# Performance work log

Hardware: AMD Instinct MI355X
Metric: run time of the kernel (lower is better)

## Reference

```python
import jax, jax.numpy as jnp
import numpy as np

B, T, C, H = 4, 2048, 1024, 16
D = C // H          # head_dim = 64
FF = 2 * C          # ff_mult = 2
EPS = 1e-5


def _layernorm(x, g, b):
    mu = jnp.mean(x, axis=-1, keepdims=True)
    var = jnp.mean((x - mu) ** 2, axis=-1, keepdims=True)
    return (x - mu) * jax.lax.rsqrt(var + EPS) * g + b


def setup_inputs() -> dict:
    key = jax.random.key(0)
    ks = jax.random.split(key, 8)
    x = jax.random.normal(ks[0], (B, T, C), dtype=jnp.float32)
    perm = jax.random.permutation(ks[1], T).astype(jnp.int32)
    s_c = 1.0 / np.sqrt(C)
    s_f = 1.0 / np.sqrt(FF)
    Wqkv = jax.random.normal(ks[2], (C, 3 * C), dtype=jnp.float32) * s_c
    Wproj = jax.random.normal(ks[3], (C, C), dtype=jnp.float32) * s_c
    bproj = jnp.zeros((C,), dtype=jnp.float32)
    ln1_g = jnp.ones((C,), dtype=jnp.float32)
    ln1_b = jnp.zeros((C,), dtype=jnp.float32)
    ln2_g = jnp.ones((C,), dtype=jnp.float32)
    ln2_b = jnp.zeros((C,), dtype=jnp.float32)
    Wff1 = jax.random.normal(ks[4], (C, FF), dtype=jnp.float32) * s_c
    bff1 = jnp.zeros((FF,), dtype=jnp.float32)
    Wff2 = jax.random.normal(ks[5], (FF, C), dtype=jnp.float32) * s_f
    bff2 = jnp.zeros((C,), dtype=jnp.float32)
    return {"x": x, "perm": perm, "Wqkv": Wqkv, "Wproj": Wproj, "bproj": bproj,
            "ln1_g": ln1_g, "ln1_b": ln1_b, "ln2_g": ln2_g, "ln2_b": ln2_b,
            "Wff1": Wff1, "bff1": bff1, "Wff2": Wff2, "bff2": bff2}


def reference(x, perm, Wqkv, Wproj, bproj, ln1_g, ln1_b, ln2_g, ln2_b,
              Wff1, bff1, Wff2, bff2):
    # --- attention branch ---
    h = _layernorm(x, ln1_g, ln1_b)                       # [B,T,C]
    qkv = (h @ Wqkv).reshape(B, T, 3, H, D)
    q, k, v = qkv[:, :, 0], qkv[:, :, 1], qkv[:, :, 2]    # [B,T,H,D]
    # random-permuted causal additive mask: masked = ~tril[:, perm]
    rows = jnp.arange(T)[:, None]
    masked = perm[None, :] > rows                          # [T,T] bool
    bias = jnp.where(masked, -jnp.inf, 0.0).astype(x.dtype)
    scale = 1.0 / np.sqrt(D)
    scores = jnp.einsum('bqhd,bkhd->bhqk', q, k) * scale + bias
    attn = jax.nn.softmax(scores, axis=-1)                 # [B,H,T,T]
    y = jnp.einsum('bhqk,bkhd->bqhd', attn, v).reshape(B, T, C)
    x = x + y @ Wproj + bproj
    # --- MLP branch ---
    h2 = _layernorm(x, ln2_g, ln2_b)
    ff = jax.nn.gelu(h2 @ Wff1 + bff1, approximate=False) @ Wff2 + bff2
    return x + ff
```

## Files before the change

### kernel.cpp

```cpp
#include <hip/hip_runtime.h>
#include <math.h>

#define Bb 4
#define Tt 2048
#define Cc 1024
#define Hh 16
#define Dd 64
#define FFf 2048
#define Mrows (Bb*Tt)

typedef _Float16 f16;
typedef _Float16 half8 __attribute__((ext_vector_type(8)));
typedef _Float16 half4 __attribute__((ext_vector_type(4)));
typedef _Float16 half2 __attribute__((ext_vector_type(2)));
typedef float floatx4 __attribute__((ext_vector_type(4)));

#define MFMA16(a,b,c)    __builtin_amdgcn_mfma_f32_16x16x32_f16(a,b,c,0,0,0)
#define MFMA16K16(a,b,c) __builtin_amdgcn_mfma_f32_16x16x16f16(a,b,c,0,0,0)

__device__ __forceinline__ void g2l16(const void* g, void* l) {
  __builtin_amdgcn_global_load_lds((__attribute__((address_space(1))) void*)(g),
                                   (__attribute__((address_space(3))) void*)(l),
                                   16, 0, 0);
}

__global__ __launch_bounds__(256) void wt_all_kernel(
    const float* __restrict__ Wqkv, const float* __restrict__ Wproj,
    const float* __restrict__ Wff1, const float* __restrict__ Wff2,
    f16* __restrict__ WqkvT, f16* __restrict__ WprojT,
    f16* __restrict__ Wff1T, f16* __restrict__ Wff2T) {
  __shared__ float tile[32][33];
  int idx = blockIdx.x;
  const float* W; f16* WT; int K, N, n0, k0;
  if (idx < 3072)      { W = Wqkv;  WT = WqkvT;  K = Cc;  N = 3*Cc; n0 = (idx % 96)*32; k0 = (idx / 96)*32; }
  else if (idx < 4096) { idx -= 3072; W = Wproj; WT = WprojT; K = Cc;  N = Cc;  n0 = (idx % 32)*32; k0 = (idx / 32)*32; }
  else if (idx < 6144) { idx -= 4096; W = Wff1;  WT = Wff1T;  K = Cc;  N = FFf; n0 = (idx % 64)*32; k0 = (idx / 64)*32; }
  else                 { idx -= 6144; W = Wff2;  WT = Wff2T;  K = FFf; N = Cc;  n0 = (idx % 32)*32; k0 = (idx / 32)*32; }
  const int tx = threadIdx.x, ty = threadIdx.y;
  #pragma unroll
  for (int i = 0; i < 4; i++)
    tile[ty + 8*i][tx] = W[(size_t)(k0 + ty + 8*i) * N + n0 + tx];
  __syncthreads();
  #pragma unroll
  for (int i = 0; i < 4; i++)
    WT[(size_t)(n0 + ty + 8*i) * K + k0 + tx] = (f16)tile[tx][ty + 8*i];
}

__global__ __launch_bounds__(256) void ln_kernel(const float* __restrict__ x,
                                                 const float* __restrict__ gam,
                                                 const float* __restrict__ bet,
                                                 f16* __restrict__ out) {
  const int row = blockIdx.x;
  const int tid = threadIdx.x;
  const float4 v = ((const float4*)(x + (size_t)row * Cc))[tid];
  float s  = v.x + v.y + v.z + v.w;
  float ss = v.x*v.x + v.y*v.y + v.z*v.z + v.w*v.w;
  #pragma unroll
  for (int o = 32; o >= 1; o >>= 1) { s += __shfl_xor(s, o); ss += __shfl_xor(ss, o); }
  __shared__ float ps[4], pss[4];
  if ((tid & 63) == 0) { ps[tid >> 6] = s; pss[tid >> 6] = ss; }
  __syncthreads();
  s  = ps[0] + ps[1] + ps[2] + ps[3];
  ss = pss[0] + pss[1] + pss[2] + pss[3];
  const float mu   = s * (1.0f / Cc);
  const float rstd = rsqrtf(ss * (1.0f / Cc) - mu * mu + 1e-5f);
  const float4 g4 = ((const float4*)gam)[tid];
  const float4 b4 = ((const float4*)bet)[tid];
  half4 o;
  o[0] = (f16)((v.x - mu) * rstd * g4.x + b4.x);
  o[1] = (f16)((v.y - mu) * rstd * g4.y + b4.y);
  o[2] = (f16)((v.z - mu) * rstd * g4.z + b4.z);
  o[3] = (f16)((v.w - mu) * rstd * g4.w + b4.w);
  ((half4*)(out + (size_t)row * Cc))[tid] = o;
}

template <int MODE>
__global__ __launch_bounds__(256, 3) void gemm_kernel(
    const f16* __restrict__ A, const f16* __restrict__ Bt, const int Kdim,
    const float* __restrict__ resid, const float* __restrict__ bias,
    float* __restrict__ outF, f16* __restrict__ outH,
    f16* __restrict__ outQ, f16* __restrict__ outK, f16* __restrict__ outV) {
  __shared__ f16 As[128 * 32];
  __shared__ f16 Bs[128 * 32];
  const int tid = threadIdx.x;
  const int lane = tid & 63;
  const int w = tid >> 6;
  const int wr = w >> 1, wc = w & 1;
  const int bm = blockIdx.y, bn = blockIdx.x;

  floatx4 acc[4][4] = {};

  const size_t aBase = (size_t)(bm*128 + w*32 + (lane >> 2)) * Kdim + (lane & 3) * 8;
  const size_t bBase = (size_t)(bn*128 + w*32 + (lane >> 2)) * Kdim + (lane & 3) * 8;

  for (int ks = 0; ks < Kdim; ks += 32) {
    __syncthreads();
    g2l16(A  + aBase + ks,                    &As[(w*2 + 0) * 512]);
    g2l16(A  + aBase + (size_t)16*Kdim + ks,  &As[(w*2 + 1) * 512]);
    g2l16(Bt + bBase + ks,                    &Bs[(w*2 + 0) * 512]);
    g2l16(Bt + bBase + (size_t)16*Kdim + ks,  &Bs[(w*2 + 1) * 512]);
    __syncthreads();
    half8 aF[4], bF[4];
    #pragma unroll
    for (int mi = 0; mi < 4; mi++)
      aF[mi] = *(const half8*)&As[(wr*64 + mi*16 + (lane & 15)) * 32 + (lane >> 4) * 8];
    #pragma unroll
    for (int ni = 0; ni < 4; ni++)
      bF[ni] = *(const half8*)&Bs[(wc*64 + ni*16 + (lane & 15)) * 32 + (lane >> 4) * 8];
    #pragma unroll
    for (int mi = 0; mi < 4; mi++)
      #pragma unroll
      for (int ni = 0; ni < 4; ni++)
        acc[mi][ni] = MFMA16(aF[mi], bF[ni], acc[mi][ni]);
  }

  const int rowBase = bm*128 + wr*64;
  const int colBase = bn*128 + wc*64;
  const int quadL = (lane >> 4);
  #pragma unroll
  for (int mi = 0; mi < 4; mi++) {
    #pragma unroll
    for (int ni = 0; ni < 4; ni++) {
      const int col = colBase + ni*16 + (lane & 15);
      if (MODE == 0) {
        const int s = col >> 10;
        const int hh = (col >> 6) & 15;
        const int d = col & 63;
        const int row0 = rowBase + mi*16 + quadL*4;
        const int bI = row0 >> 11;
        const int t0 = row0 & 2047;
        if (s == 2) {
          const size_t addr = (((size_t)(bI*Hh + hh)) * Dd + d) * Tt +
                              (t0 & ~63) + quadL*16 + ((t0 >> 4) & 3) * 4;
          half4 o;
          #pragma unroll
          for (int r = 0; r < 4; r++) o[r] = (f16)acc[mi][ni][r];
          *(half4*)&outV[addr] = o;
        } else {
          f16* dst = (s == 0) ? outQ : outK;
          const float sc = (s == 0) ? 0.18033688f : 1.0f;
          #pragma unroll
          for (int r = 0; r < 4; r++)
            dst[(((size_t)(bI*Hh + hh)) * Tt + t0 + r) * Dd + d] = (f16)(acc[mi][ni][r] * sc);
        }
      } else {
        #pragma unroll
        for (int r = 0; r < 4; r++) {
          const int row = rowBase + mi*16 + quadL*4 + r;
          const float vv = acc[mi][ni][r];
          if (MODE == 1) {
            const size_t a = (size_t)row * Cc + col;
            outF[a] = vv + resid[a] + bias[col];
          } else if (MODE == 2) {
            const float t = vv + bias[col];
            const float gl = 0.5f * t * (1.0f + erff(t * 0.70710678118654752f));
            outH[(size_t)row * FFf + col] = (f16)gl;
          } else {
            const size_t a = (size_t)row * Cc + col;
            outF[a] = vv + bias[col] + resid[a];
          }
        }
      }
    }
  }
}

__global__ __launch_bounds__(256, 4) void attn_kernel(
    const f16* __restrict__ Q, const f16* __restrict__ Kg,
    const f16* __restrict__ Vtp, const int* __restrict__ perm,
    f16* __restrict__ Y) {
  __shared__ f16 Ks[64 * 64];
  __shared__ f16 Vs[64 * 64];
  __shared__ int permS[64];

  const int tid = threadIdx.x;
  const int lane = tid & 63;
  const int w = tid >> 6;
  const int low = lane & 15;
  const int quad = lane >> 4;
  const int bh = blockIdx.y;
  const int q0 = blockIdx.x * 128;
  const int b = bh >> 4, h = bh & 15;

  half8 qF[2][2];
  {
    const size_t base = ((size_t)bh * Tt + q0 + w*32) * Dd;
    #pragma unroll
    for (int qi = 0; qi < 2; qi++)
      #pragma unroll
      for (int kc = 0; kc < 2; kc++)
        qF[qi][kc] = *(const half8*)(Q + base + (size_t)(qi*16 + low) * Dd +
                                     kc*32 + quad*8);
  }

  floatx4 O[4][2] = {};
  floatx4 Ol[2] = {};
  const half4 ones4 = {(f16)1.f, (f16)1.f, (f16)1.f, (f16)1.f};

  const int gd = ((lane & 7) ^ (lane >> 3)) * 8;
  const int krow = lane >> 3;

  for (int kt = 0; kt < Tt / 64; kt++) {
    const int kbase = kt * 64;
    __syncthreads();
    {
      const size_t kgBase = ((size_t)bh * Tt + kbase) * Dd;
      const size_t vgBase = ((size_t)bh * Dd) * Tt + kbase;
      g2l16(Kg  + kgBase + (size_t)(w*16 + 0 + krow) * Dd + gd, &Ks[(w*2 + 0) * 512]);
      g2l16(Kg  + kgBase + (size_t)(w*16 + 8 + krow) * Dd + gd, &Ks[(w*2 + 1) * 512]);
      g2l16(Vtp + vgBase + (size_t)(w*16 + 0 + krow) * Tt + gd, &Vs[(w*2 + 0) * 512]);
      g2l16(Vtp + vgBase + (size_t)(w*16 + 8 + krow) * Tt + gd, &Vs[(w*2 + 1) * 512]);
      if (tid < 64) permS[tid] = perm[kbase + tid];
    }
    __syncthreads();

    floatx4 S[2][4] = {};
    #pragma unroll
    for (int kc = 0; kc < 2; kc++) {
      #pragma unroll
      for (int ki = 0; ki < 4; ki++) {
        const int key = ki*16 + low;
        const half8 kf = *(const half8*)&Ks[key * 64 + (((kc*4 + quad) ^ (lane & 7)) * 8)];
        S[0][ki] = MFMA16(kf, qF[0][kc], S[0][ki]);
        S[1][ki] = MFMA16(kf, qF[1][kc], S[1][ki]);
      }
    }

    int4 pk[4];
    #pragma unroll
    for (int ki = 0; ki < 4; ki++) pk[ki] = *(const int4*)&permS[ki*16 + quad*4];

    half4 pF[2][4];
    #pragma unroll
    for (int qi = 0; qi < 2; qi++) {
      const int qrow = q0 + w*32 + qi*16 + low;
      #pragma unroll
      for (int ki = 0; ki < 4; ki++) {
        const floatx4 sv = S[qi][ki];
        const float p0 = (pk[ki].x > qrow) ? 0.f : __builtin_amdgcn_exp2f(sv[0]);
        const float p1 = (pk[ki].y > qrow) ? 0.f : __builtin_amdgcn_exp2f(sv[1]);
        const float p2 = (pk[ki].z > qrow) ? 0.f : __builtin_amdgcn_exp2f(sv[2]);
        const float p3 = (pk[ki].w > qrow) ? 0.f : __builtin_amdgcn_exp2f(sv[3]);
        const half2 lo = __builtin_bit_cast(half2, __builtin_amdgcn_cvt_pkrtz(p0, p1));
        const half2 hi = __builtin_bit_cast(half2, __builtin_amdgcn_cvt_pkrtz(p2, p3));
        pF[qi][ki] = __builtin_shufflevector(lo, hi, 0, 1, 2, 3);
      }
    }

    #pragma unroll
    for (int ki2 = 0; ki2 < 2; ki2++) {
      Ol[0] = MFMA16K16(ones4, pF[0][2*ki2 + 0], Ol[0]);
      Ol[1] = MFMA16K16(ones4, pF[1][2*ki2 + 0], Ol[1]);
      Ol[0] = MFMA16K16(ones4, pF[0][2*ki2 + 1], Ol[0]);
      Ol[1] = MFMA16K16(ones4, pF[1][2*ki2 + 1], Ol[1]);
      #pragma unroll
      for (int ni = 0; ni < 4; ni++) {
        const int d = ni*16 + low;
        const half8 v8 = *(const half8*)&Vs[d * 64 + (((quad*2 + ki2) ^ (lane & 7)) * 8)];
        const half4 vfA = __builtin_shufflevector(v8, v8, 0, 1, 2, 3);
        const half4 vfB = __builtin_shufflevector(v8, v8, 4, 5, 6, 7);
        O[ni][0] = MFMA16K16(vfA, pF[0][2*ki2 + 0], O[ni][0]);
        O[ni][1] = MFMA16K16(vfA, pF[1][2*ki2 + 0], O[ni][1]);
        O[ni][0] = MFMA16K16(vfB, pF[0][2*ki2 + 1], O[ni][0]);
        O[ni][1] = MFMA16K16(vfB, pF[1][2*ki2 + 1], O[ni][1]);
      }
    }
  }

  #pragma unroll
  for (int qi = 0; qi < 2; qi++) {
    const float linv = 1.0f / Ol[qi][0];
    const int trow = q0 + w*32 + qi*16 + low;
    #pragma unroll
    for (int ni = 0; ni < 4; ni++) {
      half4 o;
      #pragma unroll
      for (int r = 0; r < 4; r++) o[r] = (f16)(O[ni][qi][r] * linv);
      *(half4*)&Y[((size_t)(b * Tt + trow)) * Cc + h*64 + ni*16 + quad*4] = o;
    }
  }
}

extern "C" void kernel_launch(void* const* d_in, const int* in_sizes, int n_in,
                              void* d_out, int out_size, void* d_ws, size_t ws_size,
                              hipStream_t stream) {
  const float* x     = (const float*)d_in[0];
  const int*   perm  = (const int*)d_in[1];
  const float* Wqkv  = (const float*)d_in[2];
  const float* Wproj = (const float*)d_in[3];
  const float* bproj = (const float*)d_in[4];
  const float* ln1g  = (const float*)d_in[5];
  const float* ln1b  = (const float*)d_in[6];
  const float* ln2g  = (const float*)d_in[7];
  const float* ln2b  = (const float*)d_in[8];
  const float* Wff1  = (const float*)d_in[9];
  const float* bff1  = (const float*)d_in[10];
  const float* Wff2  = (const float*)d_in[11];
  const float* bff2  = (const float*)d_in[12];
  float* out = (float*)d_out;

  char* ws = (char*)d_ws;
  size_t off = 0;
  auto alloc = [&](size_t bytes) -> void* {
    void* p = ws + off;
    off += (bytes + 255) & ~(size_t)255;
    return p;
  };
  f16*   h1     = (f16*)alloc((size_t)Mrows * Cc * 2);
  f16*   qb     = (f16*)alloc((size_t)Mrows * Cc * 2);
  f16*   kb     = (f16*)alloc((size_t)Mrows * Cc * 2);
  f16*   vtp    = (f16*)alloc((size_t)Mrows * Cc * 2);
  f16*   yb     = (f16*)alloc((size_t)Mrows * Cc * 2);
  float* xa     = (float*)alloc((size_t)Mrows * Cc * 4);
  f16*   h2     = (f16*)alloc((size_t)Mrows * Cc * 2);
  f16*   gb     = (f16*)alloc((size_t)Mrows * FFf * 2);
  f16*   WqkvT  = (f16*)alloc((size_t)3 * Cc * Cc * 2);
  f16*   WprojT = (f16*)alloc((size_t)Cc * Cc * 2);
  f16*   Wff1T  = (f16*)alloc((size_t)FFf * Cc * 2);
  f16*   Wff2T  = (f16*)alloc((size_t)Cc * FFf * 2);

  wt_all_kernel<<<8192, dim3(32, 8), 0, stream>>>(Wqkv, Wproj, Wff1, Wff2,
                                                  WqkvT, WprojT, Wff1T, Wff2T);

  ln_kernel<<<Mrows, 256, 0, stream>>>(x, ln1g, ln1b, h1);

  gemm_kernel<0><<<dim3(3*Cc/128, Mrows/128), 256, 0, stream>>>(
      h1, WqkvT, Cc, nullptr, nullptr, nullptr, nullptr, qb, kb, vtp);

  attn_kernel<<<dim3(Tt/128, Bb*Hh), 256, 0, stream>>>(qb, kb, vtp, perm, yb);

  gemm_kernel<1><<<dim3(Cc/128, Mrows/128), 256, 0, stream>>>(
      yb, WprojT, Cc, x, bproj, xa, nullptr, nullptr, nullptr, nullptr);

  ln_kernel<<<Mrows, 256, 0, stream>>>(xa, ln2g, ln2b, h2);

  gemm_kernel<2><<<dim3(FFf/128, Mrows/128), 256, 0, stream>>>(
      h2, Wff1T, Cc, nullptr, bff1, nullptr, gb, nullptr, nullptr, nullptr);

  gemm_kernel<3><<<dim3(Cc/128, Mrows/128), 256, 0, stream>>>(
      gb, Wff2T, FFf, xa, bff2, out, nullptr, nullptr, nullptr, nullptr);
}
```

Baseline: 446.1 us.

## Switch GEMM to 32x32x16 MFMA with K=64 tiles and XOR-swizzled LDS

The GEMM kernel moves from 16x16x32 MFMA to the 32x32x16 instruction, so each wave holds a 2x2 grid of 32x32 accumulators. The K tile per iteration doubles from 32 to 64, which halves the number of barrier pairs, and the LDS layout uses an XOR swizzle on 16-byte chunks to avoid bank conflicts on fragment reads. The aim is higher MFMA throughput per LDS read and less synchronization overhead. In exchange, the kernel uses twice the LDS per block, which may cut occupancy under launch_bounds(256,3). The epilogue index mapping, including the V transpose layout, had to be rewritten and could be wrong.

```diff
diff --git a/kernel.cpp b/kernel.cpp
--- a/kernel.cpp
+++ b/kernel.cpp
@@ -14,9 +14,11 @@
 typedef _Float16 half4 __attribute__((ext_vector_type(4)));
 typedef _Float16 half2 __attribute__((ext_vector_type(2)));
 typedef float floatx4 __attribute__((ext_vector_type(4)));
+typedef float floatx16 __attribute__((ext_vector_type(16)));
 
 #define MFMA16(a,b,c)    __builtin_amdgcn_mfma_f32_16x16x32_f16(a,b,c,0,0,0)
 #define MFMA16K16(a,b,c) __builtin_amdgcn_mfma_f32_16x16x16f16(a,b,c,0,0,0)
+#define MFMA32(a,b,c)    __builtin_amdgcn_mfma_f32_32x32x16_f16(a,b,c,0,0,0)
 
 __device__ __forceinline__ void g2l16(const void* g, void* l) {
   __builtin_amdgcn_global_load_lds((__attribute__((address_space(1))) void*)(g),
@@ -80,84 +82,99 @@
     const float* __restrict__ resid, const float* __restrict__ bias,
     float* __restrict__ outF, f16* __restrict__ outH,
     f16* __restrict__ outQ, f16* __restrict__ outK, f16* __restrict__ outV) {
-  __shared__ f16 As[128 * 32];
-  __shared__ f16 Bs[128 * 32];
+  __shared__ f16 As[128 * 64];
+  __shared__ f16 Bs[128 * 64];
   const int tid = threadIdx.x;
   const int lane = tid & 63;
   const int w = tid >> 6;
   const int wr = w >> 1, wc = w & 1;
   const int bm = blockIdx.y, bn = blockIdx.x;
 
-  floatx4 acc[4][4] = {};
-
-  const size_t aBase = (size_t)(bm*128 + w*32 + (lane >> 2)) * Kdim + (lane & 3) * 8;
-  const size_t bBase = (size_t)(bn*128 + w*32 + (lane >> 2)) * Kdim + (lane & 3) * 8;
-
-  for (int ks = 0; ks < Kdim; ks += 32) {
+  floatx16 acc[2][2] = {};
+
+  const int srow = lane >> 3;
+  const int scol = ((lane & 7) ^ srow) * 8;
+  const size_t aBase = (size_t)(bm*128 + w*32 + srow) * Kdim + scol;
+  const size_t bBase = (size_t)(bn*128 + w*32 + srow) * Kdim + scol;
+
+  const int m0 = wr*64 + (lane & 31);
+  const int n0 = wc*64 + (lane & 31);
+  const int khalf = lane >> 5;
+  const int mx = (lane & 7);
+
+  for (int ks = 0; ks < Kdim; ks += 64) {
     __syncthreads();
-    g2l16(A  + aBase + ks,                    &As[(w*2 + 0) * 512]);
-    g2l16(A  + aBase + (size_t)16*Kdim + ks,  &As[(w*2 + 1) * 512]);
-    g2l16(Bt + bBase + ks,                    &Bs[(w*2 + 0) * 512]);
-    g2l16(Bt + bBase + (size_t)16*Kdim + ks,  &Bs[(w*2 + 1) * 512]);
+    #pragma unroll
+    for (int c = 0; c < 4; c++) {
+      g2l16(A  + aBase + (size_t)(c*8)*Kdim + ks, &As[(w*32 + c*8) * 64]);
+      g2l16(Bt + bBase + (size_t)(c*8)*Kdim + ks, &Bs[(w*32 + c*8) * 64]);
+    }
     __syncthreads();
-    half8 aF[4], bF[4];
-    #pragma unroll
-    for (int mi = 0; mi < 4; mi++)
-      aF[mi] = *(const half8*)&As[(wr*64 + mi*16 + (lane & 15)) * 32 + (lane >> 4) * 8];
-    #pragma unroll
-    for (int ni = 0; ni < 4; ni++)
-      bF[ni] = *(const half8*)&Bs[(wc*64 + ni*16 + (lane & 15)) * 32 + (lane >> 4) * 8];
-    #pragma unroll
-    for (int mi = 0; mi < 4; mi++)
-      #pragma unroll
-      for (int ni = 0; ni < 4; ni++)
-        acc[mi][ni] = MFMA16(aF[mi], bF[ni], acc[mi][ni]);
+    #pragma unroll
+    for (int kk = 0; kk < 4; kk++) {
+      const int kg = kk*2 + khalf;
+      half8 aF[2], bF[2];
+      aF[0] = *(const half8*)&As[(m0     ) * 64 + ((kg ^ mx) * 8)];
+      aF[1] = *(const half8*)&As[(m0 + 32) * 64 + ((kg ^ mx) * 8)];
+      bF[0] = *(const half8*)&Bs[(n0     ) * 64 + ((kg ^ mx) * 8)];
+      bF[1] = *(const half8*)&Bs[(n0 + 32) * 64 + ((kg ^ mx) * 8)];
+      acc[0][0] = MFMA32(aF[0], bF[0], acc[0][0]);
+      acc[0][1] = MFMA32(aF[0], bF[1], acc[0][1]);
+      acc[1][0] = MFMA32(aF[1], bF[0], acc[1][0]);
+      acc[1][1] = MFMA32(aF[1], bF[1], acc[1][1]);
+    }
   }
 
   const int rowBase = bm*128 + wr*64;
   const int colBase = bn*128 + wc*64;
-  const int quadL = (lane >> 4);
-  #pragma unroll
-  for (int mi = 0; mi < 4; mi++) {
-    #pragma unroll
-    for (int ni = 0; ni < 4; ni++) {
-      const int col = colBase + ni*16 + (lane & 15);
+  #pragma unroll
+  for (int mi = 0; mi < 2; mi++) {
+    #pragma unroll
+    for (int ni = 0; ni < 2; ni++) {
+      const int col = colBase + ni*32 + (lane & 31);
       if (MODE == 0) {
         const int s = col >> 10;
         const int hh = (col >> 6) & 15;
         const int d = col & 63;
-        const int row0 = rowBase + mi*16 + quadL*4;
-        const int bI = row0 >> 11;
-        const int t0 = row0 & 2047;
-        if (s == 2) {
-          const size_t addr = (((size_t)(bI*Hh + hh)) * Dd + d) * Tt +
-                              (t0 & ~63) + quadL*16 + ((t0 >> 4) & 3) * 4;
-          half4 o;
-          #pragma unroll
-          for (int r = 0; r < 4; r++) o[r] = (f16)acc[mi][ni][r];
-          *(half4*)&outV[addr] = o;
-        } else {
-          f16* dst = (s == 0) ? outQ : outK;
-          const float sc = (s == 0) ? 0.18033688f : 1.0f;
-          #pragma unroll
-          for (int r = 0; r < 4; r++)
-            dst[(((size_t)(bI*Hh + hh)) * Tt + t0 + r) * Dd + d] = (f16)(acc[mi][ni][r] * sc);
+        #pragma unroll
+        for (int g = 0; g < 4; g++) {
+          const int row0 = rowBase + mi*32 + 4*khalf + 8*g;
+          const int bI = row0 >> 11;
+          const int t0 = row0 & 2047;
+          if (s == 2) {
+            const size_t addr = (((size_t)(bI*Hh + hh)) * Dd + d) * Tt +
+                                (t0 & ~63) + ((t0 >> 2) & 3)*16 + ((t0 >> 4) & 3)*4;
+            half4 o;
+            #pragma unroll
+            for (int r = 0; r < 4; r++) o[r] = (f16)acc[mi][ni][g*4 + r];
+            *(half4*)&outV[addr] = o;
+          } else {
+            f16* dst = (s == 0) ? outQ : outK;
+            const float sc = (s == 0) ? 0.18033688f : 1.0f;
+            #pragma unroll
+            for (int r = 0; r < 4; r++)
+              dst[(((size_t)(bI*Hh + hh)) * Tt + t0 + r) * Dd + d] =
+                  (f16)(acc[mi][ni][g*4 + r] * sc);
+          }
         }
       } else {
         #pragma unroll
-        for (int r = 0; r < 4; r++) {
-          const int row = rowBase + mi*16 + quadL*4 + r;
-          const float vv = acc[mi][ni][r];
-          if (MODE == 1) {
-            const size_t a = (size_t)row * Cc + col;
-            outF[a] = vv + resid[a] + bias[col];
-          } else if (MODE == 2) {
-            const float t = vv + bias[col];
-            const float gl = 0.5f * t * (1.0f + erff(t * 0.70710678118654752f));
-            outH[(size_t)row * FFf + col] = (f16)gl;
-          } else {
-            const size_t a = (size_t)row * Cc + col;
-            outF[a] = vv + bias[col] + resid[a];
+        for (int g = 0; g < 4; g++) {
+          #pragma unroll
+          for (int r = 0; r < 4; r++) {
+            const int row = rowBase + mi*32 + 4*khalf + 8*g + r;
+            const float vv = acc[mi][ni][g*4 + r];
+            if (MODE == 1) {
+              const size_t a = (size_t)row * Cc + col;
+              outF[a] = vv + resid[a] + bias[col];
+            } else if (MODE == 2) {
+              const float t = vv + bias[col];
+              const float gl = 0.5f * t * (1.0f + erff(t * 0.70710678118654752f));
+              outH[(size_t)row * FFf + col] = (f16)gl;
+            } else {
+              const size_t a = (size_t)row * Cc + col;
+              outF[a] = vv + bias[col] + resid[a];
+            }
           }
         }
       }
```

After: 446.4 us. Within noise of the previous version (+0.1%).
